# Kernel optimization log

Measured on AMD Instinct MI355X. Metric: run time of the kernel, lower is better.

## Reference

```python
import jax, jax.numpy as jnp
import numpy as np

K_HEADS = 8
SMALL_VALUE = -32767.0  # -2**15 + 1.0


def setup_inputs() -> dict:
    key = jax.random.key(0)
    ks = jax.random.split(key, 12)
    B, Cx, Ct, N, T = 16, 256, 256, 170, 64
    c_in, c_out = Cx + Ct, 512
    s_in = 1.0 / np.sqrt(c_in)
    s_out = 1.0 / np.sqrt(c_out)
    return {
        "x": jax.random.normal(ks[0], (B, Cx, N, T), jnp.float32),
        "tem_embedding": jax.random.normal(ks[1], (B, Ct, N, T), jnp.float32),
        "Wq": jax.random.normal(ks[2], (c_out, c_in), jnp.float32) * s_in,
        "bq": jax.random.normal(ks[3], (c_out,), jnp.float32) * 0.01,
        "Wk": jax.random.normal(ks[4], (c_out, c_in), jnp.float32) * s_in,
        "bk": jax.random.normal(ks[5], (c_out,), jnp.float32) * 0.01,
        "Wv": jax.random.normal(ks[6], (c_out, c_in), jnp.float32) * s_in,
        "bv": jax.random.normal(ks[7], (c_out,), jnp.float32) * 0.01,
        "Wo": jax.random.normal(ks[8], (c_out, c_out), jnp.float32) * s_out,
        "bo": jax.random.normal(ks[9], (c_out,), jnp.float32) * 0.01,
    }


def reference(x, tem_embedding, Wq, bq, Wk, bk, Wv, bv, Wo, bo):
    T = x.shape[3]
    # concat temporal embedding (sliced to last T steps) on channel dim
    xin = jnp.concatenate([x, tem_embedding[:, :, :, -T:]], axis=1)  # [B, c_in, N, T]

    def conv1x1(W, b):
        return jnp.einsum('oc,bcnt->bont', W, xin) + b[None, :, None, None]

    q = conv1x1(Wq, bq)  # [B, c_out, N, T]
    k = conv1x1(Wk, bk)
    v = conv1x1(Wv, bv)

    B, C, N, _ = q.shape
    d = C // K_HEADS

    def heads(t):
        # torch.cat(torch.split(t, d, dim=1), dim=0): head-major batch stacking
        return jnp.transpose(t.reshape(B, K_HEADS, d, N, T), (1, 0, 3, 4, 2))  # [K,B,N,T,d]

    qh, kh, vh = heads(q), heads(k), heads(v)

    scores = jnp.einsum('kbntd,kbnsd->kbnts', qh, kh) / jnp.sqrt(jnp.float32(d))
    causal = jnp.tril(jnp.ones((T, T), dtype=bool))  # [T, T]
    scores = jnp.where(causal[None, None, None], scores, SMALL_VALUE)
    attn = jax.nn.softmax(scores, axis=-1)
    out = jnp.einsum('kbnts,kbnsd->kbntd', attn, vh)  # [K,B,N,T,d]

    # merge heads back to channel dim (head-major channel order)
    out = jnp.transpose(out, (1, 0, 4, 2, 3)).reshape(B, C, N, T)  # [B, c_out, N, T]
    y = jnp.einsum('oc,bcnt->bont', Wo, out) + bo[None, :, None, None]
    return jax.nn.relu(y)
```

## Files before the change

kernel.cpp:

```cpp
#include <hip/hip_runtime.h>
#include <cstdint>
#include <cstddef>

#define B_    16
#define N_    170
#define T_    64
#define NT_   (N_ * T_)
#define C_    512
#define KH_   8

typedef unsigned short u16;
typedef float  f32x4  __attribute__((ext_vector_type(4)));
typedef short  bf16x8 __attribute__((ext_vector_type(8)));

__device__ __forceinline__ u16 f2bf(float f) {
  union { float f; unsigned u; } v; v.f = f;
  unsigned r = v.u + 0x7fffu + ((v.u >> 16) & 1u);
  return (u16)(r >> 16);
}

#define GLDS16(g, l) \
  __builtin_amdgcn_global_load_lds((const __attribute__((address_space(1))) void*)(g), \
                                   (__attribute__((address_space(3))) void*)(l), 16, 0, 0)

__global__ __launch_bounds__(256) void wconv(const float* __restrict__ wq, const float* __restrict__ wk,
                                             const float* __restrict__ wv, const float* __restrict__ wo,
                                             u16* __restrict__ oq, u16* __restrict__ ok,
                                             u16* __restrict__ ov, u16* __restrict__ oo) {
  int idx = blockIdx.x * 256 + threadIdx.x;
  int mat = idx >> 16;
  int off = (idx & 65535) * 4;
  const float* s = (mat == 0) ? wq : (mat == 1) ? wk : (mat == 2) ? wv : wo;
  u16* d = (mat == 0) ? oq : (mat == 1) ? ok : (mat == 2) ? ov : oo;
  float4 v = *(const float4*)(s + off);
  u16 o[4] = { f2bf(v.x), f2bf(v.y), f2bf(v.z), f2bf(v.w) };
  *(uint2*)(d + off) = *(uint2*)o;
}

__global__ __launch_bounds__(256) void concat_tr(const float* __restrict__ x,
                                                 const float* __restrict__ tem,
                                                 u16* __restrict__ xin_tm) {
  __shared__ u16 tile[64 * 72];
  int mt = blockIdx.x, ct = blockIdx.y, b = blockIdx.z;
  const float* src = (ct < 4) ? (x   + ((size_t)b * 256 + (size_t)ct * 64) * NT_)
                              : (tem + ((size_t)b * 256 + (size_t)(ct - 4) * 64) * NT_);
  int m0 = mt * 64;
  int tid = threadIdx.x;
  for (int g = tid; g < 1024; g += 256) {
    int row = g >> 4, part = (g & 15) * 4;
    float4 v = *(const float4*)(src + (size_t)row * NT_ + m0 + part);
    u16* t = &tile[row * 72 + part];
    t[0] = f2bf(v.x); t[1] = f2bf(v.y); t[2] = f2bf(v.z); t[3] = f2bf(v.w);
  }
  __syncthreads();
  for (int h = tid; h < 512; h += 256) {
    int mm = h >> 3, part = (h & 7) * 8;
    u16 vals[8];
#pragma unroll
    for (int e = 0; e < 8; e++) vals[e] = tile[(part + e) * 72 + mm];
    *(uint4*)(xin_tm + ((size_t)(b * NT_ + m0 + mm)) * 512 + ct * 64 + part) = *(uint4*)vals;
  }
}

template <int MODE>
__global__ __launch_bounds__(256) void gemm_bt(
    const u16* __restrict__ A, int lda, size_t aBatch,
    const u16* __restrict__ Bm, int ldb, size_t bBatch,
    void* __restrict__ Cv, int ldc, size_t cBatch,
    const float* __restrict__ bias, int K) {
  __shared__ u16 As[128 * 32];
  __shared__ u16 Bs[128 * 32];
  int b = blockIdx.z;
  const u16* Ab = A + (size_t)b * aBatch;
  const u16* Bb = Bm + (size_t)b * bBatch;
  int tid = threadIdx.x;
  int lane = tid & 63, w = tid >> 6;
  int quad = lane >> 4, l15 = lane & 15;
  int rowA0 = blockIdx.y * 128;
  int rowB0 = blockIdx.x * 128;
  int wr = (w >> 1) * 64, wc = (w & 1) * 64;

  f32x4 acc[4][4];
#pragma unroll
  for (int i = 0; i < 4; i++)
#pragma unroll
    for (int j = 0; j < 4; j++) acc[i][j] = (f32x4){0.f, 0.f, 0.f, 0.f};

  for (int k0 = 0; k0 < K; k0 += 32) {
#pragma unroll
    for (int r = 0; r < 2; r++) {
      int chunk = tid + r * 256;
      int row = chunk >> 2, kk = (chunk & 3) * 8;
      const u16* ga = Ab + (size_t)(rowA0 + row) * lda + k0 + kk;
      GLDS16(ga, &As[(r * 256 + w * 64) * 8]);
      const u16* gb = Bb + (size_t)(rowB0 + row) * ldb + k0 + kk;
      GLDS16(gb, &Bs[(r * 256 + w * 64) * 8]);
    }
    __syncthreads();
    bf16x8 af[4], bfr[4];
#pragma unroll
    for (int i = 0; i < 4; i++) af[i]  = *(const bf16x8*)&As[(wr + i * 16 + l15) * 32 + quad * 8];
#pragma unroll
    for (int j = 0; j < 4; j++) bfr[j] = *(const bf16x8*)&Bs[(wc + j * 16 + l15) * 32 + quad * 8];
#pragma unroll
    for (int i = 0; i < 4; i++)
#pragma unroll
      for (int j = 0; j < 4; j++)
        acc[i][j] = __builtin_amdgcn_mfma_f32_16x16x32_bf16(af[i], bfr[j], acc[i][j], 0, 0, 0);
    __syncthreads();
  }

  int gr0 = rowA0 + wr, gc0 = rowB0 + wc;
  if (MODE == 0) {
    u16* C = (u16*)Cv + (size_t)b * cBatch;
#pragma unroll
    for (int j = 0; j < 4; j++) {
      int Cc = gc0 + j * 16 + l15;
      float bj = bias[Cc];
#pragma unroll
      for (int i = 0; i < 4; i++)
#pragma unroll
        for (int r = 0; r < 4; r++) {
          int R = gr0 + i * 16 + quad * 4 + r;
          C[(size_t)R * ldc + Cc] = f2bf(acc[i][j][r] + bj);
        }
    }
  } else if (MODE == 1) {
    u16* C = (u16*)Cv + (size_t)b * cBatch;
#pragma unroll
    for (int i = 0; i < 4; i++)
#pragma unroll
      for (int r = 0; r < 4; r++) {
        int R = gr0 + i * 16 + quad * 4 + r;
        float br = bias[R];
#pragma unroll
        for (int j = 0; j < 4; j++)
          C[(size_t)R * ldc + gc0 + j * 16 + l15] = f2bf(acc[i][j][r] + br);
      }
  } else {
    float* C = (float*)Cv + (size_t)b * cBatch;
#pragma unroll
    for (int i = 0; i < 4; i++)
#pragma unroll
      for (int r = 0; r < 4; r++) {
        int R = gr0 + i * 16 + quad * 4 + r;
        float br = bias[R];
#pragma unroll
        for (int j = 0; j < 4; j++) {
          float v = acc[i][j][r] + br;
          C[(size_t)R * ldc + gc0 + j * 16 + l15] = fmaxf(v, 0.f);
        }
      }
  }
}

__global__ __launch_bounds__(256) void attn(const u16* __restrict__ q_tm,
                                            const u16* __restrict__ k_tm,
                                            const u16* __restrict__ v_cm,
                                            u16* __restrict__ ao_tm) {
  __shared__ u16 qsh[64 * 72], ksh[64 * 72], vsh[64 * 72], psh[64 * 72];
  int n = blockIdx.x, kh = blockIdx.y, b = blockIdx.z;
  int tid = threadIdx.x, lane = tid & 63, w = tid >> 6;
  int quad = lane >> 4, l15 = lane & 15;

  const u16* qbase = q_tm + ((size_t)(b * NT_ + n * 64)) * 512 + kh * 64;
  const u16* kbase = k_tm + ((size_t)(b * NT_ + n * 64)) * 512 + kh * 64;
  const u16* vbase = v_cm + ((size_t)(b * 512 + kh * 64)) * NT_ + n * 64;

  for (int g = tid; g < 512; g += 256) {
    int row = g >> 3, part = (g & 7) * 8;
    *(uint4*)&qsh[row * 72 + part] = *(const uint4*)(qbase + (size_t)row * 512 + part);
    *(uint4*)&ksh[row * 72 + part] = *(const uint4*)(kbase + (size_t)row * 512 + part);
    *(uint4*)&vsh[row * 72 + part] = *(const uint4*)(vbase + (size_t)row * NT_ + part);
  }
  __syncthreads();

  f32x4 sacc[4];
#pragma unroll
  for (int j = 0; j < 4; j++) sacc[j] = (f32x4){0.f, 0.f, 0.f, 0.f};
  bf16x8 aq[2];
#pragma unroll
  for (int kc = 0; kc < 2; kc++)
    aq[kc] = *(const bf16x8*)&qsh[(w * 16 + l15) * 72 + kc * 32 + quad * 8];
#pragma unroll
  for (int j = 0; j < 4; j++)
#pragma unroll
    for (int kc = 0; kc < 2; kc++) {
      bf16x8 bk = *(const bf16x8*)&ksh[(j * 16 + l15) * 72 + kc * 32 + quad * 8];
      sacc[j] = __builtin_amdgcn_mfma_f32_16x16x32_bf16(aq[kc], bk, sacc[j], 0, 0, 0);
    }

  float pv[4][4];
#pragma unroll
  for (int r = 0; r < 4; r++) {
    int t = w * 16 + quad * 4 + r;
    float m = -3.4e38f;
#pragma unroll
    for (int j = 0; j < 4; j++) {
      int s = j * 16 + l15;
      float v = sacc[j][r] * 0.125f;
      if (s > t) v = -32767.0f;
      pv[j][r] = v;
      m = fmaxf(m, v);
    }
#pragma unroll
    for (int off = 1; off < 16; off <<= 1) m = fmaxf(m, __shfl_xor(m, off, 16));
    float sum = 0.f;
#pragma unroll
    for (int j = 0; j < 4; j++) {
      float e = __expf(pv[j][r] - m);
      pv[j][r] = e;
      sum += e;
    }
#pragma unroll
    for (int off = 1; off < 16; off <<= 1) sum += __shfl_xor(sum, off, 16);
    float inv = 1.f / sum;
#pragma unroll
    for (int j = 0; j < 4; j++)
      psh[(size_t)t * 72 + j * 16 + l15] = f2bf(pv[j][r] * inv);
  }
  f32x4 oacc[4];
#pragma unroll
  for (int j = 0; j < 4; j++) oacc[j] = (f32x4){0.f, 0.f, 0.f, 0.f};
  bf16x8 ap[2];
#pragma unroll
  for (int kc = 0; kc < 2; kc++)
    ap[kc] = *(const bf16x8*)&psh[(w * 16 + l15) * 72 + kc * 32 + quad * 8];
#pragma unroll
  for (int dj = 0; dj < 4; dj++)
#pragma unroll
    for (int kc = 0; kc < 2; kc++) {
      bf16x8 bv = *(const bf16x8*)&vsh[(dj * 16 + l15) * 72 + kc * 32 + quad * 8];
      oacc[dj] = __builtin_amdgcn_mfma_f32_16x16x32_bf16(ap[kc], bv, oacc[dj], 0, 0, 0);
    }

  u16* ob = ao_tm + ((size_t)(b * NT_ + n * 64)) * 512 + kh * 64;
#pragma unroll
  for (int dj = 0; dj < 4; dj++)
#pragma unroll
    for (int r = 0; r < 4; r++) {
      int t = w * 16 + quad * 4 + r, d = dj * 16 + l15;
      ob[(size_t)t * 512 + d] = f2bf(oacc[dj][r]);
    }
}

extern "C" void kernel_launch(void* const* d_in, const int* in_sizes, int n_in,
                              void* d_out, int out_size, void* d_ws, size_t ws_size,
                              hipStream_t stream) {
  const float* x   = (const float*)d_in[0];
  const float* tem = (const float*)d_in[1];
  const float* Wq  = (const float*)d_in[2];
  const float* bq  = (const float*)d_in[3];
  const float* Wk  = (const float*)d_in[4];
  const float* bk  = (const float*)d_in[5];
  const float* Wv  = (const float*)d_in[6];
  const float* bv  = (const float*)d_in[7];
  const float* Wo  = (const float*)d_in[8];
  const float* bo  = (const float*)d_in[9];
  float* out = (float*)d_out;

  const size_t E = (size_t)B_ * 512 * NT_;
  u16* xin_tm = (u16*)d_ws;
  u16* q_tm   = xin_tm + E;
  u16* k_tm   = q_tm + E;
  u16* v_cm   = k_tm + E;
  u16* wqb    = v_cm + E;
  u16* wkb    = wqb + 262144;
  u16* wvb    = wkb + 262144;
  u16* wob    = wvb + 262144;
  u16* ao_tm  = xin_tm;

  const size_t sBNT = (size_t)NT_ * 512;

  wconv<<<1024, 256, 0, stream>>>(Wq, Wk, Wv, Wo, wqb, wkb, wvb, wob);
  concat_tr<<<dim3(N_, 8, B_), 256, 0, stream>>>(x, tem, xin_tm);

  gemm_bt<0><<<dim3(4, 85, B_), 256, 0, stream>>>(xin_tm, 512, sBNT,
                                                  wqb, 512, (size_t)0,
                                                  q_tm, 512, sBNT, bq, 512);
  gemm_bt<0><<<dim3(4, 85, B_), 256, 0, stream>>>(xin_tm, 512, sBNT,
                                                  wkb, 512, (size_t)0,
                                                  k_tm, 512, sBNT, bk, 512);
  gemm_bt<1><<<dim3(85, 4, B_), 256, 0, stream>>>(wvb, 512, (size_t)0,
                                                  xin_tm, 512, sBNT,
                                                  v_cm, NT_, sBNT, bv, 512);
  attn<<<dim3(N_, KH_, B_), 256, 0, stream>>>(q_tm, k_tm, v_cm, ao_tm);

  gemm_bt<2><<<dim3(85, 4, B_), 256, 0, stream>>>(wob, 512, (size_t)0,
                                                  ao_tm, 512, sBNT,
                                                  out, NT_, sBNT, bo, 512);
}
```

Baseline: 1.395 ms.

## Fuse QKV projections into one GEMM with XCD-aware tile swizzle and staged stores

The three Q/K/V projection GEMMs become a single launch over a concatenated weight and bias buffer. V is now written token-major and transposed into shared memory inside the attention kernel. Block indices are remapped so neighbouring tiles land on the same XCD, improving L2 reuse of A/B tiles. The MODE 0 epilogue stages results through shared memory so global writes are 16-byte vectors. The costs are extra LDS use, an extra barrier, and scalar, bank-conflict-prone V transposes in attention.

Result: faster. 1.328 ms (-4.8%).

```diff
diff --git a/kernel.cpp b/kernel.cpp
--- a/kernel.cpp
+++ b/kernel.cpp
@@ -23,10 +23,19 @@
   __builtin_amdgcn_global_load_lds((const __attribute__((address_space(1))) void*)(g), \
                                    (__attribute__((address_space(3))) void*)(l), 16, 0, 0)
 
+__device__ __forceinline__ int xcd_swz(int orig, int n) {
+  int q = n >> 3, r = n & 7;
+  int xcd = orig & 7, idx = orig >> 3;
+  return (xcd < r ? xcd * (q + 1) : r * (q + 1) + (xcd - r) * q) + idx;
+}
+
 __global__ __launch_bounds__(256) void wconv(const float* __restrict__ wq, const float* __restrict__ wk,
                                              const float* __restrict__ wv, const float* __restrict__ wo,
+                                             const float* __restrict__ bq, const float* __restrict__ bk,
+                                             const float* __restrict__ bv,
                                              u16* __restrict__ oq, u16* __restrict__ ok,
-                                             u16* __restrict__ ov, u16* __restrict__ oo) {
+                                             u16* __restrict__ ov, u16* __restrict__ oo,
+                                             float* __restrict__ obias) {
   int idx = blockIdx.x * 256 + threadIdx.x;
   int mat = idx >> 16;
   int off = (idx & 65535) * 4;
@@ -35,6 +44,8 @@
   float4 v = *(const float4*)(s + off);
   u16 o[4] = { f2bf(v.x), f2bf(v.y), f2bf(v.z), f2bf(v.w) };
   *(uint2*)(d + off) = *(uint2*)o;
+  if (idx < 1536)
+    obias[idx] = (idx < 512) ? bq[idx] : (idx < 1024) ? bk[idx - 512] : bv[idx - 1024];
 }
 
 __global__ __launch_bounds__(256) void concat_tr(const float* __restrict__ x,
@@ -66,18 +77,26 @@
 __global__ __launch_bounds__(256) void gemm_bt(
     const u16* __restrict__ A, int lda, size_t aBatch,
     const u16* __restrict__ Bm, int ldb, size_t bBatch,
-    void* __restrict__ Cv, int ldc, size_t cBatch,
+    void* __restrict__ Cv, int ldc, size_t cBatch, size_t matStride,
     const float* __restrict__ bias, int K) {
+  constexpr int NBLK  = (MODE == 0) ? 1020 : 340;
+  constexpr int NFAST = (MODE == 0) ? 12 : 4;
   __shared__ u16 As[128 * 32];
   __shared__ u16 Bs[128 * 32];
+  __shared__ u16 cst[(MODE == 0) ? 128 * 136 : 16];
+
   int b = blockIdx.z;
+  int lin = xcd_swz(blockIdx.x, NBLK);
+  int fast = lin % NFAST, slow = lin / NFAST;
+  int bxT = (MODE == 0) ? fast : slow;
+  int ayT = (MODE == 0) ? slow : fast;
+  int rowA0 = ayT * 128, rowB0 = bxT * 128;
+
   const u16* Ab = A + (size_t)b * aBatch;
   const u16* Bb = Bm + (size_t)b * bBatch;
   int tid = threadIdx.x;
   int lane = tid & 63, w = tid >> 6;
   int quad = lane >> 4, l15 = lane & 15;
-  int rowA0 = blockIdx.y * 128;
-  int rowB0 = blockIdx.x * 128;
   int wr = (w >> 1) * 64, wc = (w & 1) * 64;
 
   f32x4 acc[4][4];
@@ -111,32 +130,30 @@
   }
 
   int gr0 = rowA0 + wr, gc0 = rowB0 + wc;
-  if (MODE == 0) {
-    u16* C = (u16*)Cv + (size_t)b * cBatch;
+  if constexpr (MODE == 0) {
+    int mat  = bxT >> 2;
+    int colb = (bxT & 3) * 128;
 #pragma unroll
     for (int j = 0; j < 4; j++) {
-      int Cc = gc0 + j * 16 + l15;
-      float bj = bias[Cc];
-#pragma unroll
-      for (int i = 0; i < 4; i++)
-#pragma unroll
-        for (int r = 0; r < 4; r++) {
-          int R = gr0 + i * 16 + quad * 4 + r;
-          C[(size_t)R * ldc + Cc] = f2bf(acc[i][j][r] + bj);
-        }
-    }
-  } else if (MODE == 1) {
-    u16* C = (u16*)Cv + (size_t)b * cBatch;
-#pragma unroll
-    for (int i = 0; i < 4; i++)
-#pragma unroll
-      for (int r = 0; r < 4; r++) {
-        int R = gr0 + i * 16 + quad * 4 + r;
-        float br = bias[R];
-#pragma unroll
-        for (int j = 0; j < 4; j++)
-          C[(size_t)R * ldc + gc0 + j * 16 + l15] = f2bf(acc[i][j][r] + br);
+      int lc = wc + j * 16 + l15;
+      float bj = bias[rowB0 + lc];
+#pragma unroll
+      for (int i = 0; i < 4; i++) {
+        int lr = wr + i * 16 + quad * 4;
+#pragma unroll
+        for (int r = 0; r < 4; r++)
+          cst[(lr + r) * 136 + lc] = f2bf(acc[i][j][r] + bj);
       }
+    }
+    __syncthreads();
+    u16* C = (u16*)Cv + (size_t)b * cBatch + (size_t)mat * matStride
+           + (size_t)rowA0 * ldc + colb;
+#pragma unroll
+    for (int it = 0; it < 8; it++) {
+      int chunk = tid + it * 256;
+      int row = chunk >> 4, cc = (chunk & 15) * 8;
+      *(uint4*)(C + (size_t)row * ldc + cc) = *(const uint4*)&cst[row * 136 + cc];
+    }
   } else {
     float* C = (float*)Cv + (size_t)b * cBatch;
 #pragma unroll
@@ -156,22 +173,26 @@
 
 __global__ __launch_bounds__(256) void attn(const u16* __restrict__ q_tm,
                                             const u16* __restrict__ k_tm,
-                                            const u16* __restrict__ v_cm,
+                                            const u16* __restrict__ v_tm,
                                             u16* __restrict__ ao_tm) {
-  __shared__ u16 qsh[64 * 72], ksh[64 * 72], vsh[64 * 72], psh[64 * 72];
+  __shared__ u16 qsh[64 * 72], ksh[64 * 72], psh[64 * 72];
+  __shared__ u16 vsh[64 * 66];
   int n = blockIdx.x, kh = blockIdx.y, b = blockIdx.z;
   int tid = threadIdx.x, lane = tid & 63, w = tid >> 6;
   int quad = lane >> 4, l15 = lane & 15;
 
   const u16* qbase = q_tm + ((size_t)(b * NT_ + n * 64)) * 512 + kh * 64;
   const u16* kbase = k_tm + ((size_t)(b * NT_ + n * 64)) * 512 + kh * 64;
-  const u16* vbase = v_cm + ((size_t)(b * 512 + kh * 64)) * NT_ + n * 64;
+  const u16* vbase = v_tm + ((size_t)(b * NT_ + n * 64)) * 512 + kh * 64;
 
   for (int g = tid; g < 512; g += 256) {
     int row = g >> 3, part = (g & 7) * 8;
     *(uint4*)&qsh[row * 72 + part] = *(const uint4*)(qbase + (size_t)row * 512 + part);
     *(uint4*)&ksh[row * 72 + part] = *(const uint4*)(kbase + (size_t)row * 512 + part);
-    *(uint4*)&vsh[row * 72 + part] = *(const uint4*)(vbase + (size_t)row * NT_ + part);
+    u16 tv[8];
+    *(uint4*)tv = *(const uint4*)(vbase + (size_t)row * 512 + part);
+#pragma unroll
+    for (int e = 0; e < 8; e++) vsh[(part + e) * 66 + row] = tv[e];
   }
   __syncthreads();
 
@@ -230,7 +251,12 @@
   for (int dj = 0; dj < 4; dj++)
 #pragma unroll
     for (int kc = 0; kc < 2; kc++) {
-      bf16x8 bv = *(const bf16x8*)&vsh[(dj * 16 + l15) * 72 + kc * 32 + quad * 8];
+      bf16x8 bv;
+      {
+        const unsigned* vp = (const unsigned*)&vsh[(dj * 16 + l15) * 66 + kc * 32 + quad * 8];
+        unsigned* bp = (unsigned*)&bv;
+        bp[0] = vp[0]; bp[1] = vp[1]; bp[2] = vp[2]; bp[3] = vp[3];
+      }
       oacc[dj] = __builtin_amdgcn_mfma_f32_16x16x32_bf16(ap[kc], bv, oacc[dj], 0, 0, 0);
     }
 
@@ -263,30 +289,25 @@
   u16* xin_tm = (u16*)d_ws;
   u16* q_tm   = xin_tm + E;
   u16* k_tm   = q_tm + E;
-  u16* v_cm   = k_tm + E;
-  u16* wqb    = v_cm + E;
-  u16* wkb    = wqb + 262144;
-  u16* wvb    = wkb + 262144;
-  u16* wob    = wvb + 262144;
+  u16* v_tm   = k_tm + E;
+  u16* wqkv   = v_tm + E;
+  u16* wob    = wqkv + 786432;
+  float* bqkv = (float*)(wob + 262144);
   u16* ao_tm  = xin_tm;
 
   const size_t sBNT = (size_t)NT_ * 512;
 
-  wconv<<<1024, 256, 0, stream>>>(Wq, Wk, Wv, Wo, wqb, wkb, wvb, wob);
+  wconv<<<1024, 256, 0, stream>>>(Wq, Wk, Wv, Wo, bq, bk, bv,
+                                  wqkv, wqkv + 262144, wqkv + 524288, wob, bqkv);
   concat_tr<<<dim3(N_, 8, B_), 256, 0, stream>>>(x, tem, xin_tm);
 
-  gemm_bt<0><<<dim3(4, 85, B_), 256, 0, stream>>>(xin_tm, 512, sBNT,
-                                                  wqb, 512, (size_t)0,
-                                                  q_tm, 512, sBNT, bq, 512);
-  gemm_bt<0><<<dim3(4, 85, B_), 256, 0, stream>>>(xin_tm, 512, sBNT,
-                                                  wkb, 512, (size_t)0,
-                                                  k_tm, 512, sBNT, bk, 512);
-  gemm_bt<1><<<dim3(85, 4, B_), 256, 0, stream>>>(wvb, 512, (size_t)0,
-                                                  xin_tm, 512, sBNT,
-                                                  v_cm, NT_, sBNT, bv, 512);
-  attn<<<dim3(N_, KH_, B_), 256, 0, stream>>>(q_tm, k_tm, v_cm, ao_tm);
-
-  gemm_bt<2><<<dim3(85, 4, B_), 256, 0, stream>>>(wob, 512, (size_t)0,
-                                                  ao_tm, 512, sBNT,
-                                                  out, NT_, sBNT, bo, 512);
-}
+  gemm_bt<0><<<dim3(1020, 1, B_), 256, 0, stream>>>(xin_tm, 512, sBNT,
+                                                    wqkv, 512, (size_t)0,
+                                                    q_tm, 512, sBNT, E, bqkv, 512);
+
+  attn<<<dim3(N_, KH_, B_), 256, 0, stream>>>(q_tm, k_tm, v_tm, ao_tm);
+
+  gemm_bt<2><<<dim3(340, 1, B_), 256, 0, stream>>>(wob, 512, (size_t)0,
+                                                   ao_tm, 512, sBNT,
+                                                   out, NT_, (size_t)512 * NT_, 0, bo, 512);
+}
```
